# Performance work log

Measured on AMD Instinct MI355X. Metric: run time of the kernel, lower is better.

## Reference

```python
import jax, jax.numpy as jnp
import numpy as np

BS, CIN, H, W = 1, 128, 448, 96
CLASSES = (8, 8, 8)
PAD = (0, 4, 4)
DIV = 1  # c3_line_div
K2 = H * CLASSES[0]                 # 3584 CondMul experts for stage 2
K3 = H * CLASSES[0] * CLASSES[1]    # 28672 CondMul experts for stage 3
C1_DIMS = [(128, 32), (32, 32), (32, 8)]
C2_DIMS = [(128, 32), (32, 32), (32, 16)]
C3_DIMS = [(128, 32), (32, 32), (32, 16)]


def _cond_mul(x, inds, w, b):
    # per-row expert gather then small matmul: [N,i] x [N,i,o] -> [N,o]
    return jnp.einsum('ni,nio->no', x, w[inds]) + b[inds]


def setup_inputs() -> dict:
    key = jax.random.key(0)
    ks = jax.random.split(key, 19)
    d = {'x_in': jax.random.normal(ks[0], (BS, CIN, H, W), jnp.float32)}
    k = 1
    for tag, dims, nexp in (('1', C1_DIMS, H), ('2', C2_DIMS, K2), ('3', C3_DIMS, K3)):
        for i, (ci, co) in enumerate(dims):
            if tag == '1':
                d['w1_%d' % i] = jax.random.normal(ks[k], (H, co, ci), jnp.float32) * 0.1
            else:
                d['w%s_%d' % (tag, i)] = jax.random.normal(ks[k], (nexp, ci, co), jnp.float32) * 0.1
            d['b%s_%d' % (tag, i)] = jax.random.normal(ks[k + 1], (nexp, co), jnp.float32) * 0.1
            k += 2
    return d


def reference(x_in, w1_0, b1_0, w1_1, b1_1, w1_2, b1_2,
              w2_0, b2_0, w2_1, b2_1, w2_2, b2_2,
              w3_0, b3_0, w3_1, b3_1, w3_2, b3_2):
    bs, cin, h, w = x_in.shape
    c12 = CLASSES[0] * CLASSES[1]
    c123 = c12 * CLASSES[2]
    lrelu = jax.nn.leaky_relu  # slope 0.01, matches F.leaky_relu default
    hoff = jnp.arange(h, dtype=jnp.int32)[None, :, None]  # [1,H,1] line offsets

    # stage 1: grouped 1x1 conv (one group per image line)
    x = jnp.transpose(x_in, (0, 2, 1, 3))  # [bs,H,C,W]
    x = lrelu(jnp.einsum('hoi,bhiw->bhow', w1_0, x) + b1_0[None, :, :, None])
    x = lrelu(jnp.einsum('hoi,bhiw->bhow', w1_1, x) + b1_1[None, :, :, None])
    x = jnp.einsum('hoi,bhiw->bhow', w1_2, x) + b1_2[None, :, :, None]  # [bs,H,cls1,W]
    inds1 = jnp.argmax(x, axis=2).astype(jnp.int32)  # [bs,H,W]
    inds1_l = (inds1 + CLASSES[0] * hoff).reshape(-1)  # [N]

    x_l = jnp.transpose(x_in, (0, 2, 3, 1)).reshape(-1, cin)  # [N,C], N=bs*H*W

    # stage 2: CondMul cascade routed by inds1
    x = lrelu(_cond_mul(x_l, inds1_l, w2_0, b2_0))
    x = lrelu(_cond_mul(x, inds1_l, w2_1, b2_1))
    x = _cond_mul(x, inds1_l, w2_2, b2_2)
    inds2 = jnp.argmax(x, axis=-1).astype(jnp.int32).reshape(bs, h, w)
    inds12 = inds1 * CLASSES[1] + (inds2 - PAD[1])
    inds12_cl = jnp.clip(inds12, 0, c12 - 1)
    inds12_l = (inds12_cl + c12 * hoff).reshape(-1)
    inds12_s = (inds12_cl + c12 * (hoff // DIV)).reshape(-1)

    # stage 3: CondMul cascade routed by inds12
    x = lrelu(_cond_mul(x_l, inds12_s, w3_0, b3_0))
    x = lrelu(_cond_mul(x, inds12_s, w3_1, b3_1))
    x3 = _cond_mul(x, inds12_l, w3_2, b3_2)  # [N, cls3+2*pad3]
    inds3 = jnp.argmax(x3, axis=-1).astype(jnp.int32).reshape(bs, h, w)

    inds123 = jnp.clip(inds12 * CLASSES[2] + (inds3 - PAD[2]), 0, c123 - 1)
    return inds123.reshape(bs, 1, h, w)
```

## Files before the change

kernel.cpp:

```cpp
#include <hip/hip_runtime.h>

#define H_ 448
#define W_ 96
#define CIN_ 128
#define HW_ (H_*W_)
#define PPB 48

__device__ __forceinline__ float lrelu(float v){ return v > 0.0f ? v : 0.01f*v; }

template<int NC>
__device__ __forceinline__ void sort_by_class(const unsigned char* s_cls, short* s_perm,
                                              int* s_cnt, int* s_off, int t)
{
    if (t < NC){
        int c = 0;
        for (int p = 0; p < PPB; p++) if (s_cls[p] == (unsigned char)t) c++;
        s_cnt[t] = c;
    }
    __syncthreads();
    if (t == 0){
        int a = 0;
        for (int c = 0; c < NC; c++){ s_off[c] = a; a += s_cnt[c]; }
    }
    __syncthreads();
    if (t < NC){
        int o = s_off[t];
        for (int p = 0; p < PPB; p++) if (s_cls[p] == (unsigned char)t) s_perm[o++] = (short)p;
    }
    __syncthreads();
}

__global__ __launch_bounds__(384, 6)
void cls3_fused(const float* __restrict__ X,
                const float* __restrict__ w1_0, const float* __restrict__ b1_0,
                const float* __restrict__ w1_1, const float* __restrict__ b1_1,
                const float* __restrict__ w1_2, const float* __restrict__ b1_2,
                const float* __restrict__ w2_0, const float* __restrict__ b2_0,
                const float* __restrict__ w2_1, const float* __restrict__ b2_1,
                const float* __restrict__ w2_2, const float* __restrict__ b2_2,
                const float* __restrict__ w3_0, const float* __restrict__ b3_0,
                const float* __restrict__ w3_1, const float* __restrict__ b3_1,
                const float* __restrict__ w3_2, const float* __restrict__ b3_2,
                int* __restrict__ out)
{
    __shared__ float s_w0[4096];
    __shared__ float s_w1[1024];
    __shared__ float s_w2[256];
    __shared__ float s_A[PPB*36];
    __shared__ float s_B[PPB*36];
    __shared__ unsigned char s_cls[PPB];
    __shared__ short s_perm[PPB];
    __shared__ int   s_raw[PPB];
    __shared__ int   s_cnt[64];
    __shared__ int   s_off[64];

    const int h  = blockIdx.x >> 1;
    const int wb = (blockIdx.x & 1) * PPB;
    const int t  = threadIdx.x;

    {
        const int w  = t % PPB;
        const int s  = t / PPB;
        const int hw = h*96 + wb + w;

        const float* g0 = w1_0 + (size_t)h*4096;
        for (int j = t; j < 4096; j += 384) s_w0[j] = g0[j];
        const float* g1 = w1_1 + (size_t)h*1024;
        for (int j = t; j < 1024; j += 384) s_w1[j] = g1[j];
        const float* g2 = w1_2 + (size_t)h*256;
        for (int j = t; j < 256; j += 384) s_w2[j] = g2[j];
        __syncthreads();

        {
            float acc[4];
            const float* bp = b1_0 + h*32 + s*4;
            #pragma unroll
            for (int k=0;k<4;k++) acc[k] = bp[k];
            #pragma unroll 4
            for (int i4=0;i4<32;i4++){
                const float x0 = X[(size_t)(4*i4+0)*HW_ + hw];
                const float x1 = X[(size_t)(4*i4+1)*HW_ + hw];
                const float x2 = X[(size_t)(4*i4+2)*HW_ + hw];
                const float x3 = X[(size_t)(4*i4+3)*HW_ + hw];
                #pragma unroll
                for (int k=0;k<4;k++){
                    const float4 q = *(const float4*)&s_w0[(s*4+k)*128 + 4*i4];
                    acc[k] += x0*q.x; acc[k] += x1*q.y; acc[k] += x2*q.z; acc[k] += x3*q.w;
                }
            }
            #pragma unroll
            for (int k=0;k<4;k++) s_A[w*33 + s*4 + k] = lrelu(acc[k]);
        }
        __syncthreads();

        {
            float acc[4];
            const float* bp = b1_1 + h*32 + s*4;
            #pragma unroll
            for (int k=0;k<4;k++) acc[k] = bp[k];
            #pragma unroll
            for (int i4=0;i4<8;i4++){
                const float x0 = s_A[w*33 + 4*i4+0];
                const float x1 = s_A[w*33 + 4*i4+1];
                const float x2 = s_A[w*33 + 4*i4+2];
                const float x3 = s_A[w*33 + 4*i4+3];
                #pragma unroll
                for (int k=0;k<4;k++){
                    const float4 q = *(const float4*)&s_w1[(s*4+k)*32 + 4*i4];
                    acc[k] += x0*q.x; acc[k] += x1*q.y; acc[k] += x2*q.z; acc[k] += x3*q.w;
                }
            }
            #pragma unroll
            for (int k=0;k<4;k++) s_B[w*33 + s*4 + k] = lrelu(acc[k]);
        }
        __syncthreads();

        {
            float acc = b1_2[h*8 + s];
            #pragma unroll
            for (int i4=0;i4<8;i4++){
                const float4 q = *(const float4*)&s_w2[s*32 + 4*i4];
                acc += s_B[w*33 + 4*i4+0]*q.x;
                acc += s_B[w*33 + 4*i4+1]*q.y;
                acc += s_B[w*33 + 4*i4+2]*q.z;
                acc += s_B[w*33 + 4*i4+3]*q.w;
            }
            s_A[w*33 + s] = acc;
        }
        __syncthreads();

        if (s == 0){
            const float* sc = &s_A[w*33];
            float best = sc[0]; int bi = 0;
            #pragma unroll
            for (int k=1;k<8;k++){ const float v = sc[k]; if (v > best){ best = v; bi = k; } }
            s_cls[w] = (unsigned char)bi;
        }
        __syncthreads();
    }

    sort_by_class<8>(s_cls, s_perm, s_cnt, s_off, t);

    const int p = t >> 3;
    const int j = t & 7;
    {
        const int sp = s_perm[p];
        const int c  = s_cls[sp];
        const long e = (long)h*8 + c;
        const int hw = h*96 + wb + sp;
        const float* W0 = w2_0 + e*4096 + j*4;
        const float* W1 = w2_1 + e*1024 + j*4;
        const float* W2 = w2_2 + e*512  + j*2;

        float4 acc = *(const float4*)&b2_0[e*32 + j*4];
        #pragma unroll 8
        for (int i=0;i<128;i++){
            const float xv = X[(size_t)i*HW_ + hw];
            const float4 q = *(const float4*)&W0[i*32];
            acc.x += xv*q.x; acc.y += xv*q.y; acc.z += xv*q.z; acc.w += xv*q.w;
        }
        *(float4*)&s_A[p*36 + j*4] = make_float4(lrelu(acc.x),lrelu(acc.y),lrelu(acc.z),lrelu(acc.w));
        __syncthreads();

        float4 ac2 = *(const float4*)&b2_1[e*32 + j*4];
        #pragma unroll 8
        for (int i=0;i<32;i++){
            const float xv = s_A[p*36 + i];
            const float4 q = *(const float4*)&W1[i*32];
            ac2.x += xv*q.x; ac2.y += xv*q.y; ac2.z += xv*q.z; ac2.w += xv*q.w;
        }
        *(float4*)&s_B[p*36 + j*4] = make_float4(lrelu(ac2.x),lrelu(ac2.y),lrelu(ac2.z),lrelu(ac2.w));
        __syncthreads();

        float2 sc = *(const float2*)&b2_2[e*16 + j*2];
        #pragma unroll 8
        for (int i=0;i<32;i++){
            const float xv = s_B[p*36 + i];
            const float2 r = *(const float2*)&W2[i*16];
            sc.x += xv*r.x; sc.y += xv*r.y;
        }
        float best = sc.x; int bi = j*2;
        if (sc.y > best){ best = sc.y; bi = j*2+1; }
        #pragma unroll
        for (int off=1; off<8; off<<=1){
            const float ob = __shfl_xor(best, off, 64);
            const int  obi = __shfl_xor(bi,  off, 64);
            if (ob > best || (ob == best && obi < bi)){ best = ob; bi = obi; }
        }
        __syncthreads();
        if (j == 0){
            const int raw = c*8 + bi - 4;
            s_raw[sp] = raw;
            s_cls[sp] = (unsigned char)(raw < 0 ? 0 : (raw > 63 ? 63 : raw));
        }
        __syncthreads();
    }

    sort_by_class<64>(s_cls, s_perm, s_cnt, s_off, t);

    {
        const int sp = s_perm[p];
        const int c  = s_cls[sp];
        const long e = (long)h*64 + c;
        const int hw = h*96 + wb + sp;
        const float* W0 = w3_0 + e*4096 + j*4;
        const float* W1 = w3_1 + e*1024 + j*4;
        const float* W2 = w3_2 + e*512  + j*2;

        float4 acc = *(const float4*)&b3_0[e*32 + j*4];
        #pragma unroll 8
        for (int i=0;i<128;i++){
            const float xv = X[(size_t)i*HW_ + hw];
            const float4 q = *(const float4*)&W0[i*32];
            acc.x += xv*q.x; acc.y += xv*q.y; acc.z += xv*q.z; acc.w += xv*q.w;
        }
        *(float4*)&s_A[p*36 + j*4] = make_float4(lrelu(acc.x),lrelu(acc.y),lrelu(acc.z),lrelu(acc.w));
        __syncthreads();

        float4 ac2 = *(const float4*)&b3_1[e*32 + j*4];
        #pragma unroll 8
        for (int i=0;i<32;i++){
            const float xv = s_A[p*36 + i];
            const float4 q = *(const float4*)&W1[i*32];
            ac2.x += xv*q.x; ac2.y += xv*q.y; ac2.z += xv*q.z; ac2.w += xv*q.w;
        }
        *(float4*)&s_B[p*36 + j*4] = make_float4(lrelu(ac2.x),lrelu(ac2.y),lrelu(ac2.z),lrelu(ac2.w));
        __syncthreads();

        float2 sc = *(const float2*)&b3_2[e*16 + j*2];
        #pragma unroll 8
        for (int i=0;i<32;i++){
            const float xv = s_B[p*36 + i];
            const float2 r = *(const float2*)&W2[i*16];
            sc.x += xv*r.x; sc.y += xv*r.y;
        }
        float best = sc.x; int bi = j*2;
        if (sc.y > best){ best = sc.y; bi = j*2+1; }
        #pragma unroll
        for (int off=1; off<8; off<<=1){
            const float ob = __shfl_xor(best, off, 64);
            const int  obi = __shfl_xor(bi,  off, 64);
            if (ob > best || (ob == best && obi < bi)){ best = ob; bi = obi; }
        }
        if (j == 0){
            int v = s_raw[sp]*8 + bi - 4;
            v = v < 0 ? 0 : (v > 511 ? 511 : v);
            out[h*96 + wb + sp] = v;
        }
    }
}

extern "C" void kernel_launch(void* const* d_in, const int* in_sizes, int n_in,
                              void* d_out, int out_size, void* d_ws, size_t ws_size,
                              hipStream_t stream) {
    const float* X    = (const float*)d_in[0];
    const float* w1_0 = (const float*)d_in[1];
    const float* b1_0 = (const float*)d_in[2];
    const float* w1_1 = (const float*)d_in[3];
    const float* b1_1 = (const float*)d_in[4];
    const float* w1_2 = (const float*)d_in[5];
    const float* b1_2 = (const float*)d_in[6];
    const float* w2_0 = (const float*)d_in[7];
    const float* b2_0 = (const float*)d_in[8];
    const float* w2_1 = (const float*)d_in[9];
    const float* b2_1 = (const float*)d_in[10];
    const float* w2_2 = (const float*)d_in[11];
    const float* b2_2 = (const float*)d_in[12];
    const float* w3_0 = (const float*)d_in[13];
    const float* b3_0 = (const float*)d_in[14];
    const float* w3_1 = (const float*)d_in[15];
    const float* b3_1 = (const float*)d_in[16];
    const float* w3_2 = (const float*)d_in[17];
    const float* b3_2 = (const float*)d_in[18];
    int* out = (int*)d_out;

    cls3_fused<<<H_*2, 384, 0, stream>>>(X,
        w1_0, b1_0, w1_1, b1_1, w1_2, b1_2,
        w2_0, b2_0, w2_1, b2_1, w2_2, b2_2,
        w3_0, b3_0, w3_1, b3_1, w3_2, b3_2,
        out);
}
```

Measured before the change: 152.5 us.

## Process full image line per block and prefetch expert weights into cache

Each block now handles one full line of 96 pixels with 768 threads instead of two half-line blocks. While half the threads load stage-1 weights, the other half touch all stage-2 expert weights for that line, warming the cache. After the stage-3 sort, the block touches the weights of every stage-3 expert actually used. Stage-1 work is done by 384 threads computing 8 outputs each. The aim is to cut repeated weight fetches across paired blocks and hide gather latency, at the cost of half as many blocks, larger blocks and extra register pressure.

```diff
diff --git a/kernel.cpp b/kernel.cpp
--- a/kernel.cpp
+++ b/kernel.cpp
@@ -4,7 +4,6 @@
 #define W_ 96
 #define CIN_ 128
 #define HW_ (H_*W_)
-#define PPB 48
 
 __device__ __forceinline__ float lrelu(float v){ return v > 0.0f ? v : 0.01f*v; }
 
@@ -14,7 +13,7 @@
 {
     if (t < NC){
         int c = 0;
-        for (int p = 0; p < PPB; p++) if (s_cls[p] == (unsigned char)t) c++;
+        for (int p = 0; p < 96; p++) if (s_cls[p] == (unsigned char)t) c++;
         s_cnt[t] = c;
     }
     __syncthreads();
@@ -25,12 +24,12 @@
     __syncthreads();
     if (t < NC){
         int o = s_off[t];
-        for (int p = 0; p < PPB; p++) if (s_cls[p] == (unsigned char)t) s_perm[o++] = (short)p;
+        for (int p = 0; p < 96; p++) if (s_cls[p] == (unsigned char)t) s_perm[o++] = (short)p;
     }
     __syncthreads();
 }
 
-__global__ __launch_bounds__(384, 6)
+__global__ __launch_bounds__(768, 6)
 void cls3_fused(const float* __restrict__ X,
                 const float* __restrict__ w1_0, const float* __restrict__ b1_0,
                 const float* __restrict__ w1_1, const float* __restrict__ b1_1,
@@ -46,36 +45,48 @@
     __shared__ float s_w0[4096];
     __shared__ float s_w1[1024];
     __shared__ float s_w2[256];
-    __shared__ float s_A[PPB*36];
-    __shared__ float s_B[PPB*36];
-    __shared__ unsigned char s_cls[PPB];
-    __shared__ short s_perm[PPB];
-    __shared__ int   s_raw[PPB];
+    __shared__ float s_A[96*36];
+    __shared__ float s_B[96*36];
+    __shared__ unsigned char s_cls[96];
+    __shared__ unsigned char s_cls2[96];
+    __shared__ short s_perm[96];
+    __shared__ int   s_raw[96];
     __shared__ int   s_cnt[64];
     __shared__ int   s_off[64];
 
-    const int h  = blockIdx.x >> 1;
-    const int wb = (blockIdx.x & 1) * PPB;
+    const int h  = blockIdx.x;
     const int t  = threadIdx.x;
 
     {
-        const int w  = t % PPB;
-        const int s  = t / PPB;
-        const int hw = h*96 + wb + w;
-
-        const float* g0 = w1_0 + (size_t)h*4096;
-        for (int j = t; j < 4096; j += 384) s_w0[j] = g0[j];
-        const float* g1 = w1_1 + (size_t)h*1024;
-        for (int j = t; j < 1024; j += 384) s_w1[j] = g1[j];
-        const float* g2 = w1_2 + (size_t)h*256;
-        for (int j = t; j < 256; j += 384) s_w2[j] = g2[j];
-        __syncthreads();
-
-        {
-            float acc[4];
-            const float* bp = b1_0 + h*32 + s*4;
-            #pragma unroll
-            for (int k=0;k<4;k++) acc[k] = bp[k];
+        const int w  = t % 96;
+        const int s  = t / 96;
+        const int hw = h*96 + w;
+
+        if (t < 384){
+            const float* g0 = w1_0 + (size_t)h*4096;
+            for (int j = t; j < 4096; j += 384) s_w0[j] = g0[j];
+            const float* g1 = w1_1 + (size_t)h*1024;
+            for (int j = t; j < 1024; j += 384) s_w1[j] = g1[j];
+            const float* g2 = w1_2 + (size_t)h*256;
+            for (int j = t; j < 256; j += 384) s_w2[j] = g2[j];
+        } else {
+            const int tt = t - 384;
+            float keep = 0.f;
+            const float4* p0 = (const float4*)(w2_0 + (size_t)h*32768);
+            for (int v = tt; v < 8192; v += 384){ const float4 q = p0[v]; keep += q.x+q.y+q.z+q.w; }
+            const float4* p1 = (const float4*)(w2_1 + (size_t)h*8192);
+            for (int v = tt; v < 2048; v += 384){ const float4 q = p1[v]; keep += q.x+q.y+q.z+q.w; }
+            const float4* p2 = (const float4*)(w2_2 + (size_t)h*4096);
+            for (int v = tt; v < 1024; v += 384){ const float4 q = p2[v]; keep += q.x+q.y+q.z+q.w; }
+            asm volatile("" :: "v"(keep));
+        }
+        __syncthreads();
+
+        if (t < 384){
+            float acc[8];
+            const float* bp = b1_0 + h*32 + s*8;
+            #pragma unroll
+            for (int k=0;k<8;k++) acc[k] = bp[k];
             #pragma unroll 4
             for (int i4=0;i4<32;i4++){
                 const float x0 = X[(size_t)(4*i4+0)*HW_ + hw];
@@ -83,21 +94,21 @@
                 const float x2 = X[(size_t)(4*i4+2)*HW_ + hw];
                 const float x3 = X[(size_t)(4*i4+3)*HW_ + hw];
                 #pragma unroll
-                for (int k=0;k<4;k++){
-                    const float4 q = *(const float4*)&s_w0[(s*4+k)*128 + 4*i4];
+                for (int k=0;k<8;k++){
+                    const float4 q = *(const float4*)&s_w0[(s*8+k)*128 + 4*i4];
                     acc[k] += x0*q.x; acc[k] += x1*q.y; acc[k] += x2*q.z; acc[k] += x3*q.w;
                 }
             }
             #pragma unroll
-            for (int k=0;k<4;k++) s_A[w*33 + s*4 + k] = lrelu(acc[k]);
-        }
-        __syncthreads();
-
-        {
-            float acc[4];
-            const float* bp = b1_1 + h*32 + s*4;
-            #pragma unroll
-            for (int k=0;k<4;k++) acc[k] = bp[k];
+            for (int k=0;k<8;k++) s_A[w*33 + s*8 + k] = lrelu(acc[k]);
+        }
+        __syncthreads();
+
+        if (t < 384){
+            float acc[8];
+            const float* bp = b1_1 + h*32 + s*8;
+            #pragma unroll
+            for (int k=0;k<8;k++) acc[k] = bp[k];
             #pragma unroll
             for (int i4=0;i4<8;i4++){
                 const float x0 = s_A[w*33 + 4*i4+0];
@@ -105,36 +116,43 @@
                 const float x2 = s_A[w*33 + 4*i4+2];
                 const float x3 = s_A[w*33 + 4*i4+3];
                 #pragma unroll
-                for (int k=0;k<4;k++){
-                    const float4 q = *(const float4*)&s_w1[(s*4+k)*32 + 4*i4];
+                for (int k=0;k<8;k++){
+                    const float4 q = *(const float4*)&s_w1[(s*8+k)*32 + 4*i4];
                     acc[k] += x0*q.x; acc[k] += x1*q.y; acc[k] += x2*q.z; acc[k] += x3*q.w;
                 }
             }
             #pragma unroll
-            for (int k=0;k<4;k++) s_B[w*33 + s*4 + k] = lrelu(acc[k]);
-        }
-        __syncthreads();
-
-        {
-            float acc = b1_2[h*8 + s];
+            for (int k=0;k<8;k++) s_B[w*33 + s*8 + k] = lrelu(acc[k]);
+        }
+        __syncthreads();
+
+        if (t < 384){
+            float acc[2];
+            const float* bp = b1_2 + h*8 + s*2;
+            acc[0] = bp[0]; acc[1] = bp[1];
             #pragma unroll
             for (int i4=0;i4<8;i4++){
-                const float4 q = *(const float4*)&s_w2[s*32 + 4*i4];
-                acc += s_B[w*33 + 4*i4+0]*q.x;
-                acc += s_B[w*33 + 4*i4+1]*q.y;
-                acc += s_B[w*33 + 4*i4+2]*q.z;
-                acc += s_B[w*33 + 4*i4+3]*q.w;
+                const float x0 = s_B[w*33 + 4*i4+0];
+                const float x1 = s_B[w*33 + 4*i4+1];
+                const float x2 = s_B[w*33 + 4*i4+2];
+                const float x3 = s_B[w*33 + 4*i4+3];
+                #pragma unroll
+                for (int k=0;k<2;k++){
+                    const float4 q = *(const float4*)&s_w2[(s*2+k)*32 + 4*i4];
+                    acc[k] += x0*q.x; acc[k] += x1*q.y; acc[k] += x2*q.z; acc[k] += x3*q.w;
+                }
             }
-            s_A[w*33 + s] = acc;
-        }
-        __syncthreads();
-
-        if (s == 0){
-            const float* sc = &s_A[w*33];
+            s_A[w*33 + s*2 + 0] = acc[0];
+            s_A[w*33 + s*2 + 1] = acc[1];
+        }
+        __syncthreads();
+
+        if (t < 96){
+            const float* sc = &s_A[t*33];
             float best = sc[0]; int bi = 0;
             #pragma unroll
             for (int k=1;k<8;k++){ const float v = sc[k]; if (v > best){ best = v; bi = k; } }
-            s_cls[w] = (unsigned char)bi;
+            s_cls[t] = (unsigned char)bi;
         }
         __syncthreads();
     }
@@ -147,7 +165,7 @@
         const int sp = s_perm[p];
         const int c  = s_cls[sp];
         const long e = (long)h*8 + c;
-        const int hw = h*96 + wb + sp;
+        const int hw = h*96 + sp;
         const float* W0 = w2_0 + e*4096 + j*4;
         const float* W1 = w2_1 + e*1024 + j*4;
         const float* W2 = w2_2 + e*512  + j*2;
@@ -190,19 +208,34 @@
         __syncthreads();
         if (j == 0){
             const int raw = c*8 + bi - 4;
-            s_raw[sp] = raw;
-            s_cls[sp] = (unsigned char)(raw < 0 ? 0 : (raw > 63 ? 63 : raw));
-        }
-        __syncthreads();
-    }
-
-    sort_by_class<64>(s_cls, s_perm, s_cnt, s_off, t);
+            s_raw[sp]  = raw;
+            s_cls2[sp] = (unsigned char)(raw < 0 ? 0 : (raw > 63 ? 63 : raw));
+        }
+        __syncthreads();
+    }
+
+    sort_by_class<64>(s_cls2, s_perm, s_cnt, s_off, t);
+
+    {
+        float keep = 0.f;
+        for (int c = 0; c < 64; c++){
+            if (s_cnt[c] == 0) continue;
+            const long e = (long)h*64 + c;
+            const float4* p0 = (const float4*)(w3_0 + e*4096);
+            for (int v = t; v < 1024; v += 768){ const float4 q = p0[v]; keep += q.x+q.y+q.z+q.w; }
+            const float4* p1 = (const float4*)(w3_1 + e*1024);
+            if (t < 256){ const float4 q = p1[t]; keep += q.x+q.y+q.z+q.w; }
+            const float4* p2 = (const float4*)(w3_2 + e*512);
+            if (t < 128){ const float4 q = p2[t]; keep += q.x+q.y+q.z+q.w; }
+        }
+        asm volatile("" :: "v"(keep));
+    }
 
     {
         const int sp = s_perm[p];
-        const int c  = s_cls[sp];
+        const int c  = s_cls2[sp];
         const long e = (long)h*64 + c;
-        const int hw = h*96 + wb + sp;
+        const int hw = h*96 + sp;
         const float* W0 = w3_0 + e*4096 + j*4;
         const float* W1 = w3_1 + e*1024 + j*4;
         const float* W2 = w3_2 + e*512  + j*2;
@@ -245,7 +278,7 @@
         if (j == 0){
             int v = s_raw[sp]*8 + bi - 4;
             v = v < 0 ? 0 : (v > 511 ? 511 : v);
-            out[h*96 + wb + sp] = v;
+            out[h*96 + sp] = v;
         }
     }
 }
@@ -274,7 +307,7 @@
     const float* b3_2 = (const float*)d_in[18];
     int* out = (int*)d_out;
 
-    cls3_fused<<<H_*2, 384, 0, stream>>>(X,
+    cls3_fused<<<H_, 768, 0, stream>>>(X,
         w1_0, b1_0, w1_1, b1_1, w1_2, b1_2,
         w2_0, b2_0, w2_1, b2_1, w2_2, b2_2,
         w3_0, b3_0, w3_1, b3_1, w3_2, b3_2,
```

Result: slower. 184.6 us (+21.0%).

## Split fused kernel into three per-stage kernels with byte intermediates

Applied to the files above, without the earlier changes.

Splits the single fused three-stage kernel into three kernels that pass per-pixel class indices through workspace as bytes. Each kernel uses less shared memory, so more blocks can be resident. Block indices are also remapped so that consecutive blocks cover interleaved lines, which changes L2 locality and the scheduling order. The cost is two extra launches, small global round-trips and an extra read of X per stage kernel from global memory or cache.

```diff
diff --git a/kernel.cpp b/kernel.cpp
--- a/kernel.cpp
+++ b/kernel.cpp
@@ -1,12 +1,17 @@
 #include <hip/hip_runtime.h>
 
 #define H_ 448
-#define W_ 96
 #define CIN_ 128
-#define HW_ (H_*W_)
+#define HW_ (448*96)
 #define PPB 48
 
 __device__ __forceinline__ float lrelu(float v){ return v > 0.0f ? v : 0.01f*v; }
+
+__device__ __forceinline__ void decode_block(int d, int& h, int& wb){
+    const int r = d & 15, q = d >> 4;
+    h  = (r & 7) + (q << 3);
+    wb = (r >> 3) * PPB;
+}
 
 template<int NC>
 __device__ __forceinline__ void sort_by_class(const unsigned char* s_cls, short* s_perm,
@@ -30,223 +35,244 @@
     __syncthreads();
 }
 
-__global__ __launch_bounds__(384, 6)
-void cls3_fused(const float* __restrict__ X,
-                const float* __restrict__ w1_0, const float* __restrict__ b1_0,
-                const float* __restrict__ w1_1, const float* __restrict__ b1_1,
-                const float* __restrict__ w1_2, const float* __restrict__ b1_2,
-                const float* __restrict__ w2_0, const float* __restrict__ b2_0,
-                const float* __restrict__ w2_1, const float* __restrict__ b2_1,
-                const float* __restrict__ w2_2, const float* __restrict__ b2_2,
-                const float* __restrict__ w3_0, const float* __restrict__ b3_0,
-                const float* __restrict__ w3_1, const float* __restrict__ b3_1,
-                const float* __restrict__ w3_2, const float* __restrict__ b3_2,
-                int* __restrict__ out)
+__global__ __launch_bounds__(384, 4)
+void k1_stage1(const float* __restrict__ X,
+               const float* __restrict__ w1_0, const float* __restrict__ b1_0,
+               const float* __restrict__ w1_1, const float* __restrict__ b1_1,
+               const float* __restrict__ w1_2, const float* __restrict__ b1_2,
+               unsigned char* __restrict__ inds1)
 {
     __shared__ float s_w0[4096];
     __shared__ float s_w1[1024];
     __shared__ float s_w2[256];
+    __shared__ float s_A[PPB*33];
+    __shared__ float s_B[PPB*33];
+
+    int h, wb; decode_block(blockIdx.x, h, wb);
+    const int t  = threadIdx.x;
+    const int w  = t % PPB;
+    const int s  = t / PPB;
+    const int hw = h*96 + wb + w;
+
+    const float* g0 = w1_0 + (size_t)h*4096;
+    for (int j = t; j < 4096; j += 384) s_w0[j] = g0[j];
+    const float* g1 = w1_1 + (size_t)h*1024;
+    for (int j = t; j < 1024; j += 384) s_w1[j] = g1[j];
+    const float* g2 = w1_2 + (size_t)h*256;
+    for (int j = t; j < 256; j += 384) s_w2[j] = g2[j];
+    __syncthreads();
+
+    {
+        float acc[4];
+        const float* bp = b1_0 + h*32 + s*4;
+        #pragma unroll
+        for (int k=0;k<4;k++) acc[k] = bp[k];
+        #pragma unroll 4
+        for (int i4=0;i4<32;i4++){
+            const float x0 = X[(size_t)(4*i4+0)*HW_ + hw];
+            const float x1 = X[(size_t)(4*i4+1)*HW_ + hw];
+            const float x2 = X[(size_t)(4*i4+2)*HW_ + hw];
+            const float x3 = X[(size_t)(4*i4+3)*HW_ + hw];
+            #pragma unroll
+            for (int k=0;k<4;k++){
+                const float4 q = *(const float4*)&s_w0[(s*4+k)*128 + 4*i4];
+                acc[k] += x0*q.x; acc[k] += x1*q.y; acc[k] += x2*q.z; acc[k] += x3*q.w;
+            }
+        }
+        #pragma unroll
+        for (int k=0;k<4;k++) s_A[w*33 + s*4 + k] = lrelu(acc[k]);
+    }
+    __syncthreads();
+
+    {
+        float acc[4];
+        const float* bp = b1_1 + h*32 + s*4;
+        #pragma unroll
+        for (int k=0;k<4;k++) acc[k] = bp[k];
+        #pragma unroll
+        for (int i4=0;i4<8;i4++){
+            const float x0 = s_A[w*33 + 4*i4+0];
+            const float x1 = s_A[w*33 + 4*i4+1];
+            const float x2 = s_A[w*33 + 4*i4+2];
+            const float x3 = s_A[w*33 + 4*i4+3];
+            #pragma unroll
+            for (int k=0;k<4;k++){
+                const float4 q = *(const float4*)&s_w1[(s*4+k)*32 + 4*i4];
+                acc[k] += x0*q.x; acc[k] += x1*q.y; acc[k] += x2*q.z; acc[k] += x3*q.w;
+            }
+        }
+        #pragma unroll
+        for (int k=0;k<4;k++) s_B[w*33 + s*4 + k] = lrelu(acc[k]);
+    }
+    __syncthreads();
+
+    {
+        float acc = b1_2[h*8 + s];
+        #pragma unroll
+        for (int i4=0;i4<8;i4++){
+            const float4 q = *(const float4*)&s_w2[s*32 + 4*i4];
+            acc += s_B[w*33 + 4*i4+0]*q.x;
+            acc += s_B[w*33 + 4*i4+1]*q.y;
+            acc += s_B[w*33 + 4*i4+2]*q.z;
+            acc += s_B[w*33 + 4*i4+3]*q.w;
+        }
+        s_A[w*33 + s] = acc;
+    }
+    __syncthreads();
+
+    if (s == 0){
+        const float* sc = &s_A[w*33];
+        float best = sc[0]; int bi = 0;
+        #pragma unroll
+        for (int k=1;k<8;k++){ const float v = sc[k]; if (v > best){ best = v; bi = k; } }
+        inds1[hw] = (unsigned char)bi;
+    }
+}
+
+__global__ __launch_bounds__(384, 4)
+void k2_stage2(const float* __restrict__ X,
+               const float* __restrict__ w0, const float* __restrict__ b0,
+               const float* __restrict__ w1, const float* __restrict__ b1,
+               const float* __restrict__ w2, const float* __restrict__ b2,
+               const unsigned char* __restrict__ inds1,
+               signed char* __restrict__ raw12, unsigned char* __restrict__ cls2)
+{
     __shared__ float s_A[PPB*36];
     __shared__ float s_B[PPB*36];
     __shared__ unsigned char s_cls[PPB];
     __shared__ short s_perm[PPB];
-    __shared__ int   s_raw[PPB];
+    __shared__ int   s_cnt[8];
+    __shared__ int   s_off[8];
+
+    int h, wb; decode_block(blockIdx.x, h, wb);
+    const int t = threadIdx.x;
+    if (t < PPB) s_cls[t] = inds1[h*96 + wb + t];
+    __syncthreads();
+    sort_by_class<8>(s_cls, s_perm, s_cnt, s_off, t);
+
+    const int p = t >> 3;
+    const int j = t & 7;
+    const int sp = s_perm[p];
+    const int c  = s_cls[sp];
+    const long e = (long)h*8 + c;
+    const int hw = h*96 + wb + sp;
+    const float* W0 = w0 + e*4096 + j*4;
+    const float* W1 = w1 + e*1024 + j*4;
+    const float* W2 = w2 + e*512  + j*2;
+
+    float4 acc = *(const float4*)&b0[e*32 + j*4];
+    #pragma unroll 8
+    for (int i=0;i<128;i++){
+        const float xv = X[(size_t)i*HW_ + hw];
+        const float4 q = *(const float4*)&W0[i*32];
+        acc.x += xv*q.x; acc.y += xv*q.y; acc.z += xv*q.z; acc.w += xv*q.w;
+    }
+    *(float4*)&s_A[p*36 + j*4] = make_float4(lrelu(acc.x),lrelu(acc.y),lrelu(acc.z),lrelu(acc.w));
+    __syncthreads();
+
+    float4 ac2 = *(const float4*)&b1[e*32 + j*4];
+    #pragma unroll 8
+    for (int i=0;i<32;i++){
+        const float xv = s_A[p*36 + i];
+        const float4 q = *(const float4*)&W1[i*32];
+        ac2.x += xv*q.x; ac2.y += xv*q.y; ac2.z += xv*q.z; ac2.w += xv*q.w;
+    }
+    *(float4*)&s_B[p*36 + j*4] = make_float4(lrelu(ac2.x),lrelu(ac2.y),lrelu(ac2.z),lrelu(ac2.w));
+    __syncthreads();
+
+    float2 sc = *(const float2*)&b2[e*16 + j*2];
+    #pragma unroll 8
+    for (int i=0;i<32;i++){
+        const float xv = s_B[p*36 + i];
+        const float2 r = *(const float2*)&W2[i*16];
+        sc.x += xv*r.x; sc.y += xv*r.y;
+    }
+    float best = sc.x; int bi = j*2;
+    if (sc.y > best){ best = sc.y; bi = j*2+1; }
+    #pragma unroll
+    for (int off=1; off<8; off<<=1){
+        const float ob = __shfl_xor(best, off, 64);
+        const int  obi = __shfl_xor(bi,  off, 64);
+        if (ob > best || (ob == best && obi < bi)){ best = ob; bi = obi; }
+    }
+    if (j == 0){
+        const int raw = c*8 + bi - 4;
+        raw12[hw] = (signed char)raw;
+        cls2[hw]  = (unsigned char)(raw < 0 ? 0 : (raw > 63 ? 63 : raw));
+    }
+}
+
+__global__ __launch_bounds__(384, 4)
+void k3_stage3(const float* __restrict__ X,
+               const float* __restrict__ w0, const float* __restrict__ b0,
+               const float* __restrict__ w1, const float* __restrict__ b1,
+               const float* __restrict__ w2, const float* __restrict__ b2,
+               const unsigned char* __restrict__ cls2,
+               const signed char* __restrict__ raw12,
+               int* __restrict__ out)
+{
+    __shared__ float s_A[PPB*36];
+    __shared__ float s_B[PPB*36];
+    __shared__ unsigned char s_cls[PPB];
+    __shared__ short s_perm[PPB];
     __shared__ int   s_cnt[64];
     __shared__ int   s_off[64];
 
-    const int h  = blockIdx.x >> 1;
-    const int wb = (blockIdx.x & 1) * PPB;
-    const int t  = threadIdx.x;
-
-    {
-        const int w  = t % PPB;
-        const int s  = t / PPB;
-        const int hw = h*96 + wb + w;
-
-        const float* g0 = w1_0 + (size_t)h*4096;
-        for (int j = t; j < 4096; j += 384) s_w0[j] = g0[j];
-        const float* g1 = w1_1 + (size_t)h*1024;
-        for (int j = t; j < 1024; j += 384) s_w1[j] = g1[j];
-        const float* g2 = w1_2 + (size_t)h*256;
-        for (int j = t; j < 256; j += 384) s_w2[j] = g2[j];
-        __syncthreads();
-
-        {
-            float acc[4];
-            const float* bp = b1_0 + h*32 + s*4;
-            #pragma unroll
-            for (int k=0;k<4;k++) acc[k] = bp[k];
-            #pragma unroll 4
-            for (int i4=0;i4<32;i4++){
-                const float x0 = X[(size_t)(4*i4+0)*HW_ + hw];
-                const float x1 = X[(size_t)(4*i4+1)*HW_ + hw];
-                const float x2 = X[(size_t)(4*i4+2)*HW_ + hw];
-                const float x3 = X[(size_t)(4*i4+3)*HW_ + hw];
-                #pragma unroll
-                for (int k=0;k<4;k++){
-                    const float4 q = *(const float4*)&s_w0[(s*4+k)*128 + 4*i4];
-                    acc[k] += x0*q.x; acc[k] += x1*q.y; acc[k] += x2*q.z; acc[k] += x3*q.w;
-                }
-            }
-            #pragma unroll
-            for (int k=0;k<4;k++) s_A[w*33 + s*4 + k] = lrelu(acc[k]);
-        }
-        __syncthreads();
-
-        {
-            float acc[4];
-            const float* bp = b1_1 + h*32 + s*4;
-            #pragma unroll
-            for (int k=0;k<4;k++) acc[k] = bp[k];
-            #pragma unroll
-            for (int i4=0;i4<8;i4++){
-                const float x0 = s_A[w*33 + 4*i4+0];
-                const float x1 = s_A[w*33 + 4*i4+1];
-                const float x2 = s_A[w*33 + 4*i4+2];
-                const float x3 = s_A[w*33 + 4*i4+3];
-                #pragma unroll
-                for (int k=0;k<4;k++){
-                    const float4 q = *(const float4*)&s_w1[(s*4+k)*32 + 4*i4];
-                    acc[k] += x0*q.x; acc[k] += x1*q.y; acc[k] += x2*q.z; acc[k] += x3*q.w;
-                }
-            }
-            #pragma unroll
-            for (int k=0;k<4;k++) s_B[w*33 + s*4 + k] = lrelu(acc[k]);
-        }
-        __syncthreads();
-
-        {
-            float acc = b1_2[h*8 + s];
-            #pragma unroll
-            for (int i4=0;i4<8;i4++){
-                const float4 q = *(const float4*)&s_w2[s*32 + 4*i4];
-                acc += s_B[w*33 + 4*i4+0]*q.x;
-                acc += s_B[w*33 + 4*i4+1]*q.y;
-                acc += s_B[w*33 + 4*i4+2]*q.z;
-                acc += s_B[w*33 + 4*i4+3]*q.w;
-            }
-            s_A[w*33 + s] = acc;
-        }
-        __syncthreads();
-
-        if (s == 0){
-            const float* sc = &s_A[w*33];
-            float best = sc[0]; int bi = 0;
-            #pragma unroll
-            for (int k=1;k<8;k++){ const float v = sc[k]; if (v > best){ best = v; bi = k; } }
-            s_cls[w] = (unsigned char)bi;
-        }
-        __syncthreads();
-    }
-
-    sort_by_class<8>(s_cls, s_perm, s_cnt, s_off, t);
+    int h, wb; decode_block(blockIdx.x, h, wb);
+    const int t = threadIdx.x;
+    if (t < PPB) s_cls[t] = cls2[h*96 + wb + t];
+    __syncthreads();
+    sort_by_class<64>(s_cls, s_perm, s_cnt, s_off, t);
 
     const int p = t >> 3;
     const int j = t & 7;
-    {
-        const int sp = s_perm[p];
-        const int c  = s_cls[sp];
-        const long e = (long)h*8 + c;
-        const int hw = h*96 + wb + sp;
-        const float* W0 = w2_0 + e*4096 + j*4;
-        const float* W1 = w2_1 + e*1024 + j*4;
-        const float* W2 = w2_2 + e*512  + j*2;
-
-        float4 acc = *(const float4*)&b2_0[e*32 + j*4];
-        #pragma unroll 8
-        for (int i=0;i<128;i++){
-            const float xv = X[(size_t)i*HW_ + hw];
-            const float4 q = *(const float4*)&W0[i*32];
-            acc.x += xv*q.x; acc.y += xv*q.y; acc.z += xv*q.z; acc.w += xv*q.w;
-        }
-        *(float4*)&s_A[p*36 + j*4] = make_float4(lrelu(acc.x),lrelu(acc.y),lrelu(acc.z),lrelu(acc.w));
-        __syncthreads();
-
-        float4 ac2 = *(const float4*)&b2_1[e*32 + j*4];
-        #pragma unroll 8
-        for (int i=0;i<32;i++){
-            const float xv = s_A[p*36 + i];
-            const float4 q = *(const float4*)&W1[i*32];
-            ac2.x += xv*q.x; ac2.y += xv*q.y; ac2.z += xv*q.z; ac2.w += xv*q.w;
-        }
-        *(float4*)&s_B[p*36 + j*4] = make_float4(lrelu(ac2.x),lrelu(ac2.y),lrelu(ac2.z),lrelu(ac2.w));
-        __syncthreads();
-
-        float2 sc = *(const float2*)&b2_2[e*16 + j*2];
-        #pragma unroll 8
-        for (int i=0;i<32;i++){
-            const float xv = s_B[p*36 + i];
-            const float2 r = *(const float2*)&W2[i*16];
-            sc.x += xv*r.x; sc.y += xv*r.y;
-        }
-        float best = sc.x; int bi = j*2;
-        if (sc.y > best){ best = sc.y; bi = j*2+1; }
-        #pragma unroll
-        for (int off=1; off<8; off<<=1){
-            const float ob = __shfl_xor(best, off, 64);
-            const int  obi = __shfl_xor(bi,  off, 64);
-            if (ob > best || (ob == best && obi < bi)){ best = ob; bi = obi; }
-        }
-        __syncthreads();
-        if (j == 0){
-            const int raw = c*8 + bi - 4;
-            s_raw[sp] = raw;
-            s_cls[sp] = (unsigned char)(raw < 0 ? 0 : (raw > 63 ? 63 : raw));
-        }
-        __syncthreads();
-    }
-
-    sort_by_class<64>(s_cls, s_perm, s_cnt, s_off, t);
-
-    {
-        const int sp = s_perm[p];
-        const int c  = s_cls[sp];
-        const long e = (long)h*64 + c;
-        const int hw = h*96 + wb + sp;
-        const float* W0 = w3_0 + e*4096 + j*4;
-        const float* W1 = w3_1 + e*1024 + j*4;
-        const float* W2 = w3_2 + e*512  + j*2;
-
-        float4 acc = *(const float4*)&b3_0[e*32 + j*4];
-        #pragma unroll 8
-        for (int i=0;i<128;i++){
-            const float xv = X[(size_t)i*HW_ + hw];
-            const float4 q = *(const float4*)&W0[i*32];
-            acc.x += xv*q.x; acc.y += xv*q.y; acc.z += xv*q.z; acc.w += xv*q.w;
-        }
-        *(float4*)&s_A[p*36 + j*4] = make_float4(lrelu(acc.x),lrelu(acc.y),lrelu(acc.z),lrelu(acc.w));
-        __syncthreads();
-
-        float4 ac2 = *(const float4*)&b3_1[e*32 + j*4];
-        #pragma unroll 8
-        for (int i=0;i<32;i++){
-            const float xv = s_A[p*36 + i];
-            const float4 q = *(const float4*)&W1[i*32];
-            ac2.x += xv*q.x; ac2.y += xv*q.y; ac2.z += xv*q.z; ac2.w += xv*q.w;
-        }
-        *(float4*)&s_B[p*36 + j*4] = make_float4(lrelu(ac2.x),lrelu(ac2.y),lrelu(ac2.z),lrelu(ac2.w));
-        __syncthreads();
-
-        float2 sc = *(const float2*)&b3_2[e*16 + j*2];
-        #pragma unroll 8
-        for (int i=0;i<32;i++){
-            const float xv = s_B[p*36 + i];
-            const float2 r = *(const float2*)&W2[i*16];
-            sc.x += xv*r.x; sc.y += xv*r.y;
-        }
-        float best = sc.x; int bi = j*2;
-        if (sc.y > best){ best = sc.y; bi = j*2+1; }
-        #pragma unroll
-        for (int off=1; off<8; off<<=1){
-            const float ob = __shfl_xor(best, off, 64);
-            const int  obi = __shfl_xor(bi,  off, 64);
-            if (ob > best || (ob == best && obi < bi)){ best = ob; bi = obi; }
-        }
-        if (j == 0){
-            int v = s_raw[sp]*8 + bi - 4;
-            v = v < 0 ? 0 : (v > 511 ? 511 : v);
-            out[h*96 + wb + sp] = v;
-        }
+    const int sp = s_perm[p];
+    const int c  = s_cls[sp];
+    const long e = (long)h*64 + c;
+    const int hw = h*96 + wb + sp;
+    const float* W0 = w0 + e*4096 + j*4;
+    const float* W1 = w1 + e*1024 + j*4;
+    const float* W2 = w2 + e*512  + j*2;
+
+    float4 acc = *(const float4*)&b0[e*32 + j*4];
+    #pragma unroll 8
+    for (int i=0;i<128;i++){
+        const float xv = X[(size_t)i*HW_ + hw];
+        const float4 q = *(const float4*)&W0[i*32];
+        acc.x += xv*q.x; acc.y += xv*q.y; acc.z += xv*q.z; acc.w += xv*q.w;
+    }
+    *(float4*)&s_A[p*36 + j*4] = make_float4(lrelu(acc.x),lrelu(acc.y),lrelu(acc.z),lrelu(acc.w));
+    __syncthreads();
+
+    float4 ac2 = *(const float4*)&b1[e*32 + j*4];
+    #pragma unroll 8
+    for (int i=0;i<32;i++){
+        const float xv = s_A[p*36 + i];
+        const float4 q = *(const float4*)&W1[i*32];
+        ac2.x += xv*q.x; ac2.y += xv*q.y; ac2.z += xv*q.z; ac2.w += xv*q.w;
+    }
+    *(float4*)&s_B[p*36 + j*4] = make_float4(lrelu(ac2.x),lrelu(ac2.y),lrelu(ac2.z),lrelu(ac2.w));
+    __syncthreads();
+
+    float2 sc = *(const float2*)&b2[e*16 + j*2];
+    #pragma unroll 8
+    for (int i=0;i<32;i++){
+        const float xv = s_B[p*36 + i];
+        const float2 r = *(const float2*)&W2[i*16];
+        sc.x += xv*r.x; sc.y += xv*r.y;
+    }
+    float best = sc.x; int bi = j*2;
+    if (sc.y > best){ best = sc.y; bi = j*2+1; }
+    #pragma unroll
+    for (int off=1; off<8; off<<=1){
+        const float ob = __shfl_xor(best, off, 64);
+        const int  obi = __shfl_xor(bi,  off, 64);
+        if (ob > best || (ob == best && obi < bi)){ best = ob; bi = obi; }
+    }
+    if (j == 0){
+        int v = (int)raw12[hw]*8 + bi - 4;
+        v = v < 0 ? 0 : (v > 511 ? 511 : v);
+        out[hw] = v;
     }
 }
 
@@ -274,9 +300,11 @@
     const float* b3_2 = (const float*)d_in[18];
     int* out = (int*)d_out;
 
-    cls3_fused<<<H_*2, 384, 0, stream>>>(X,
-        w1_0, b1_0, w1_1, b1_1, w1_2, b1_2,
-        w2_0, b2_0, w2_1, b2_1, w2_2, b2_2,
-        w3_0, b3_0, w3_1, b3_1, w3_2, b3_2,
-        out);
-}
+    unsigned char* inds1 = (unsigned char*)d_ws;
+    unsigned char* cls2  = inds1 + HW_;
+    signed char*   raw12 = (signed char*)(cls2 + HW_);
+
+    k1_stage1<<<H_*2, 384, 0, stream>>>(X, w1_0, b1_0, w1_1, b1_1, w1_2, b1_2, inds1);
+    k2_stage2<<<H_*2, 384, 0, stream>>>(X, w2_0, b2_0, w2_1, b2_1, w2_2, b2_2, inds1, raw12, cls2);
+    k3_stage3<<<H_*2, 384, 0, stream>>>(X, w3_0, b3_0, w3_1, b3_1, w3_2, b3_2, cls2, raw12, out);
+}
```

Result: no change. 155.4 us (+1.9%).
